# Kernel optimization log

Measured on AMD Instinct MI355X. Metric: run time of the kernel, lower is better.

Reference implementation:

```python
import jax, jax.numpy as jnp
import numpy as np

AMP = 2                      # matches init kwarg `amp`
K = 2 * AMP + 1              # kernel_size


def _offsets():
    # torch: arange(-s//2+1, s//2+1) with s=2*amp+1 -> [-amp, ..., amp]
    vec = jnp.arange(-AMP, AMP + 1, dtype=jnp.float32)
    gi, gj, gs = jnp.meshgrid(vec, vec, vec, indexing='ij')
    # reshape order matches the i-major / j / s-minor loop order below
    return jnp.stack([gi, gj, gs], axis=-1).reshape(K ** 3, 3)  # (K^3, 3)


def setup_inputs() -> dict:
    key = jax.random.key(0)
    k1, k2 = jax.random.split(key)
    B, C, H, W, D = 2, 32, 48, 48, 48
    return {
        "x_q": jax.random.normal(k1, (B, C, H, W, D), dtype=jnp.float32),
        "x_k": jax.random.normal(k2, (B, C, H, W, D), dtype=jnp.float32),
        "num_heads": 4,
    }


def reference(x_q, x_k, num_heads):
    B, C, H, W, D = x_q.shape
    hd = C // num_heads
    scale = hd ** (-0.5)
    q = x_q.reshape(B, hd, num_heads, H, W, D) * scale
    k = x_k.reshape(B, hd, num_heads, H, W, D)

    pad = [(0, 0)] * 3 + [(AMP, AMP)] * 3
    kp = jnp.pad(k, pad)  # zero pad spatial dims by amp
    # validity mask: True inside the original volume, False in the padding
    valid = jnp.pad(jnp.ones((H, W, D), dtype=bool), [(AMP, AMP)] * 3)

    attn = []
    for i in range(K):
        for j in range(K):
            for s in range(K):
                ks = kp[:, :, :, i:i + H, j:j + W, s:s + D]
                # dot over head_dim channel c -> (B, nh, H, W, D)
                a = jnp.einsum('bchxyz,bchxyz->bhxyz', q, ks)
                m = valid[i:i + H, j:j + W, s:s + D]
                attn.append(jnp.where(m, a, jnp.float32(-1000.0)))
    attn = jnp.stack(attn, axis=1)          # (B, K^3, nh, H, W, D)
    attn = jax.nn.softmax(attn, axis=1)     # softmax over the K^3 shifts

    v = _offsets()                          # (K^3, 3)
    v_ = jnp.einsum('bnhxyz,nd->bdhxyz', attn, v)  # (B, 3, nh, H, W, D)
    return jnp.mean(v_, axis=2)             # (B, 3, H, W, D)
```

## Files before the change

### kernel.cpp

```cpp
#include <hip/hip_runtime.h>


#define S_PLANE 2304
#define S_CHAN 110592
#define TOTAL  7077888

typedef _Float16 h2 __attribute__((ext_vector_type(2)));

__device__ __forceinline__ float dot2(h2 a, h2 b, float c) {
#if __has_builtin(__builtin_amdgcn_fdot2)
    return __builtin_amdgcn_fdot2(a, b, c, false);
#else
    return fmaf((float)a[0], (float)b[0], fmaf((float)a[1], (float)b[1], c));
#endif
}

__device__ __forceinline__ float fexp2(float x) {
#if __has_builtin(__builtin_amdgcn_exp2f)
    return __builtin_amdgcn_exp2f(x);
#else
    return __exp2f(x);
#endif
}

__device__ __forceinline__ h2 bc(unsigned w) { return __builtin_bit_cast(h2, w); }

__device__ __forceinline__ unsigned pkz(float a, float b) {
#if __has_builtin(__builtin_amdgcn_cvt_pkrtz)
    return __builtin_bit_cast(unsigned, __builtin_amdgcn_cvt_pkrtz(a, b));
#else
    return __builtin_bit_cast(unsigned, h2{(_Float16)a, (_Float16)b});
#endif
}

__global__ __launch_bounds__(256, 8) void mov3d_kernel(
    const float* __restrict__ xq, const float* __restrict__ xk,
    float* __restrict__ out)
{
    __shared__ __align__(16) unsigned kw[4608];

    const int tid = threadIdx.x;
    const int tz8 = tid & 7;
    const int ty = (tid >> 3) & 7;
    const int tx = tid >> 6;

    const int bid = blockIdx.x;
    int blk = (bid & 7) * 432 + (bid >> 3);

    const int h = blk / 864;
    int rem = blk - h * 864;
    const int zt = rem % 6;  rem /= 6;
    const int yt = rem % 6;  rem /= 6;
    const int xt = rem % 12;
    const int b  = rem / 12;

    const int x0 = xt * 4, y0 = yt * 8, z0 = zt * 8;
    const int x = x0 + tx, y = y0 + ty, z = z0 + tz8;
    const unsigned sp = (unsigned)(x * S_PLANE + y * 48 + z);
    const int bbase = b * (32 * S_CHAN);

    const float QSCALE = 0.35355339059327373f * 1.4426950408889634f;

    const float qf0 = xq[(unsigned)(bbase + (h     ) * S_CHAN) + sp];
    const float qf1 = xq[(unsigned)(bbase + (h +  4) * S_CHAN) + sp];
    const float qf2 = xq[(unsigned)(bbase + (h +  8) * S_CHAN) + sp];
    const float qf3 = xq[(unsigned)(bbase + (h + 12) * S_CHAN) + sp];
    const float qf4 = xq[(unsigned)(bbase + (h + 16) * S_CHAN) + sp];
    const float qf5 = xq[(unsigned)(bbase + (h + 20) * S_CHAN) + sp];
    const float qf6 = xq[(unsigned)(bbase + (h + 24) * S_CHAN) + sp];
    const float qf7 = xq[(unsigned)(bbase + (h + 28) * S_CHAN) + sp];
    const h2 qA0 = h2{(_Float16)(qf0 * QSCALE), (_Float16)(qf1 * QSCALE)};
    const h2 qA1 = h2{(_Float16)(qf2 * QSCALE), (_Float16)(qf3 * QSCALE)};
    const h2 qA2 = h2{(_Float16)(qf4 * QSCALE), (_Float16)(qf5 * QSCALE)};
    const h2 qA3 = h2{(_Float16)(qf6 * QSCALE), (_Float16)(qf7 * QSCALE)};

    const int sBase = bbase + h * S_CHAN;
#define STAGE_GROUP(G) do {                                                   \
        const int u = (G) * 256 + tid;                                        \
        if ((G) < 2 || tid < 64) {                                            \
            const int lx  = u / 72;                                           \
            const int r   = u - lx * 72;                                      \
            const int lz2 = r / 12;                                           \
            const int ly  = r - lz2 * 12;                                     \
            const int srel0 = (x0 - 2 + lx) * S_PLANE                         \
                            + (y0 - 2 + ly) * 48 + (z0 - 2 + 2 * lz2);        \
            const int srel = min(max(srel0, 0), S_CHAN - 2);                  \
            const int f = sBase + srel;     \
            const float2 vA0 = *(const float2*)&xk[f];                        \
            const float2 vA1 = *(const float2*)&xk[f +  8 * S_CHAN];          \
            const float2 vA2 = *(const float2*)&xk[f + 16 * S_CHAN];          \
            const float2 vA3 = *(const float2*)&xk[f + 24 * S_CHAN];          \
            const float2 vB0 = *(const float2*)&xk[f +  4 * S_CHAN];          \
            const float2 vB1 = *(const float2*)&xk[f + 12 * S_CHAN];          \
            const float2 vB2 = *(const float2*)&xk[f + 20 * S_CHAN];          \
            const float2 vB3 = *(const float2*)&xk[f + 28 * S_CHAN];          \
            const uint4 W0 = {pkz(vA0.x, vB0.x), pkz(vA1.x, vB1.x),           \
                              pkz(vA2.x, vB2.x), pkz(vA3.x, vB3.x)};          \
            const uint4 W1 = {pkz(vA0.y, vB0.y), pkz(vA1.y, vB1.y),           \
                              pkz(vA2.y, vB2.y), pkz(vA3.y, vB3.y)};          \
            const int L0 = lx * 144 + lz2 * 24 + ly;                          \
            *(uint4*)&kw[L0 * 4] = W0;                                        \
            *(uint4*)&kw[(L0 + 12) * 4] = W1;                                 \
        }                                                                     \
    } while (0)
    STAGE_GROUP(0);
    STAGE_GROUP(1);
    STAGE_GROUP(2);
#undef STAGE_GROUP
    __syncthreads();

    const float NEG = -16384.f;
    const float zs0 = ((unsigned)(z - 2) < 48u) ? 0.f : NEG;
    const float zs1 = ((unsigned)(z - 1) < 48u) ? 0.f : NEG;
    const float zs2 = 0.f;
    const float zs3 = ((unsigned)(z + 1) < 48u) ? 0.f : NEG;
    const float zs4 = ((unsigned)(z + 2) < 48u) ? 0.f : NEG;

    float l = 0.f, ax = 0.f, ay = 0.f, az = 0.f;

#define SCORE(T, SEED) \
    dot2(qA0, bc((T).x), dot2(qA1, bc((T).y), dot2(qA2, bc((T).z), dot2(qA3, bc((T).w), (SEED)))))

    __builtin_amdgcn_s_setprio(1);
#pragma unroll
    for (int dx = -2; dx <= 2; ++dx) {
        const bool vx = (unsigned)(x + dx) < 48u;
        const float fdx = (float)dx;
        float wsdx = 0.f;
#pragma unroll
        for (int dy = -2; dy <= 2; ++dy) {
            const bool vxy = vx && ((unsigned)(y + dy) < 48u);
            const float fdy = (float)dy;
            const unsigned* pb = kw
                + ((tx + 2 + dx) * 144 + tz8 * 12 + (ty + 2 + dy)) * 4;

            const uint4 T0 = *(const uint4*)(pb);
            const uint4 T1 = *(const uint4*)(pb + 48);
            const uint4 T2 = *(const uint4*)(pb + 96);
            const uint4 T3 = *(const uint4*)(pb + 144);
            const uint4 T4 = *(const uint4*)(pb + 192);

            const float e0 = fexp2(SCORE(T0, zs0));
            const float e1 = fexp2(SCORE(T1, zs1));
            const float e2 = fexp2(SCORE(T2, zs2));
            const float e3 = fexp2(SCORE(T3, zs3));
            const float e4 = fexp2(SCORE(T4, zs4));

            float ws  = ((e0 + e1) + (e2 + e3)) + e4;
            float azP = fmaf(2.f, e4 - e0, e3 - e1);

            ws  = vxy ? ws  : 0.f;
            azP = vxy ? azP : 0.f;

            wsdx += ws;
            ay = fmaf(fdy, ws, ay);
            az += azP;
        }
        ax = fmaf(fdx, wsdx, ax);
        l += wsdx;
    }
    __builtin_amdgcn_s_setprio(0);
#undef SCORE

    const float r = 0.25f / l;
    const unsigned ob = (unsigned)b * (3 * S_CHAN);
    atomicAdd(&out[ob + 0u * S_CHAN + sp], ax * r);
    atomicAdd(&out[ob + 1u * S_CHAN + sp], ay * r);
    atomicAdd(&out[ob + 2u * S_CHAN + sp], az * r);
}

extern "C" void kernel_launch(void* const* d_in, const int* in_sizes, int n_in,
                              void* d_out, int out_size, void* d_ws, size_t ws_size,
                              hipStream_t stream) {
    const float* xq = (const float*)d_in[0];
    const float* xk = (const float*)d_in[1];
    float* out = (float*)d_out;
    hipMemsetAsync(out, 0, (size_t)out_size * sizeof(float), stream);
    mov3d_kernel<<<3456, 256, 0, stream>>>(xq, xk, out);
}
```

Baseline: 50.43 us.

## Compute two z-outputs per thread and enlarge tile to 8x8x8 with padded LDS

Each thread now computes two adjacent z voxels, so the six staged key rows serve both outputs and LDS reads per output drop. The block tile grows from 4x8x8 to 8x8x8, which lowers the share of staged halo per output and halves the grid. The LDS row stride is padded from 144 to 145 to reduce bank conflicts. In exchange it uses more LDS and registers per block (launch bounds lowered to 5 blocks), so occupancy falls and fewer blocks cover the GPU.

Measured after the change: 65.45 us. 29.8% more time.

```diff
diff --git a/kernel.cpp b/kernel.cpp
--- a/kernel.cpp
+++ b/kernel.cpp
@@ -33,51 +33,55 @@
 #endif
 }
 
-__global__ __launch_bounds__(256, 8) void mov3d_kernel(
+__global__ __launch_bounds__(256, 5) void mov3d_kernel(
     const float* __restrict__ xq, const float* __restrict__ xk,
     float* __restrict__ out)
 {
-    __shared__ __align__(16) unsigned kw[4608];
+    __shared__ __align__(16) unsigned kw[6960];
 
     const int tid = threadIdx.x;
-    const int tz8 = tid & 7;
-    const int ty = (tid >> 3) & 7;
-    const int tx = tid >> 6;
+    const int tzi = tid & 3;
+    const int ty = (tid >> 2) & 7;
+    const int tx = tid >> 5;
 
     const int bid = blockIdx.x;
-    int blk = (bid & 7) * 432 + (bid >> 3);
-
-    const int h = blk / 864;
-    int rem = blk - h * 864;
-    const int zt = rem % 6;  rem /= 6;
-    const int yt = rem % 6;  rem /= 6;
-    const int xt = rem % 12;
-    const int b  = rem / 12;
-
-    const int x0 = xt * 4, y0 = yt * 8, z0 = zt * 8;
-    const int x = x0 + tx, y = y0 + ty, z = z0 + tz8;
-    const unsigned sp = (unsigned)(x * S_PLANE + y * 48 + z);
+    int blk = (bid & 7) * 216 + (bid >> 3);
+
+    const int h = blk / 432;
+    int rem = blk - h * 432;
+    const int b = rem / 216;  rem -= b * 216;
+    const int xt = rem / 36;  rem -= xt * 36;
+    const int yt = rem / 6;
+    const int zt = rem - yt * 6;
+
+    const int x0 = xt * 8, y0 = yt * 8, z0 = zt * 8;
+    const int x = x0 + tx, y = y0 + ty, zA = z0 + 2 * tzi;
+    const unsigned sp = (unsigned)(x * S_PLANE + y * 48 + zA);
     const int bbase = b * (32 * S_CHAN);
 
     const float QSCALE = 0.35355339059327373f * 1.4426950408889634f;
 
-    const float qf0 = xq[(unsigned)(bbase + (h     ) * S_CHAN) + sp];
-    const float qf1 = xq[(unsigned)(bbase + (h +  4) * S_CHAN) + sp];
-    const float qf2 = xq[(unsigned)(bbase + (h +  8) * S_CHAN) + sp];
-    const float qf3 = xq[(unsigned)(bbase + (h + 12) * S_CHAN) + sp];
-    const float qf4 = xq[(unsigned)(bbase + (h + 16) * S_CHAN) + sp];
-    const float qf5 = xq[(unsigned)(bbase + (h + 20) * S_CHAN) + sp];
-    const float qf6 = xq[(unsigned)(bbase + (h + 24) * S_CHAN) + sp];
-    const float qf7 = xq[(unsigned)(bbase + (h + 28) * S_CHAN) + sp];
-    const h2 qA0 = h2{(_Float16)(qf0 * QSCALE), (_Float16)(qf1 * QSCALE)};
-    const h2 qA1 = h2{(_Float16)(qf2 * QSCALE), (_Float16)(qf3 * QSCALE)};
-    const h2 qA2 = h2{(_Float16)(qf4 * QSCALE), (_Float16)(qf5 * QSCALE)};
-    const h2 qA3 = h2{(_Float16)(qf6 * QSCALE), (_Float16)(qf7 * QSCALE)};
+    const float2 qf0 = *(const float2*)&xq[(unsigned)(bbase + (h     ) * S_CHAN) + sp];
+    const float2 qf1 = *(const float2*)&xq[(unsigned)(bbase + (h +  4) * S_CHAN) + sp];
+    const float2 qf2 = *(const float2*)&xq[(unsigned)(bbase + (h +  8) * S_CHAN) + sp];
+    const float2 qf3 = *(const float2*)&xq[(unsigned)(bbase + (h + 12) * S_CHAN) + sp];
+    const float2 qf4 = *(const float2*)&xq[(unsigned)(bbase + (h + 16) * S_CHAN) + sp];
+    const float2 qf5 = *(const float2*)&xq[(unsigned)(bbase + (h + 20) * S_CHAN) + sp];
+    const float2 qf6 = *(const float2*)&xq[(unsigned)(bbase + (h + 24) * S_CHAN) + sp];
+    const float2 qf7 = *(const float2*)&xq[(unsigned)(bbase + (h + 28) * S_CHAN) + sp];
+    const h2 qA0 = h2{(_Float16)(qf0.x * QSCALE), (_Float16)(qf1.x * QSCALE)};
+    const h2 qA1 = h2{(_Float16)(qf2.x * QSCALE), (_Float16)(qf3.x * QSCALE)};
+    const h2 qA2 = h2{(_Float16)(qf4.x * QSCALE), (_Float16)(qf5.x * QSCALE)};
+    const h2 qA3 = h2{(_Float16)(qf6.x * QSCALE), (_Float16)(qf7.x * QSCALE)};
+    const h2 qB0 = h2{(_Float16)(qf0.y * QSCALE), (_Float16)(qf1.y * QSCALE)};
+    const h2 qB1 = h2{(_Float16)(qf2.y * QSCALE), (_Float16)(qf3.y * QSCALE)};
+    const h2 qB2 = h2{(_Float16)(qf4.y * QSCALE), (_Float16)(qf5.y * QSCALE)};
+    const h2 qB3 = h2{(_Float16)(qf6.y * QSCALE), (_Float16)(qf7.y * QSCALE)};
 
     const int sBase = bbase + h * S_CHAN;
 #define STAGE_GROUP(G) do {                                                   \
         const int u = (G) * 256 + tid;                                        \
-        if ((G) < 2 || tid < 64) {                                            \
+        if ((G) < 3 || tid < 96) {                                            \
             const int lx  = u / 72;                                           \
             const int r   = u - lx * 72;                                      \
             const int lz2 = r / 12;                                           \
@@ -98,75 +102,95 @@
                               pkz(vA2.x, vB2.x), pkz(vA3.x, vB3.x)};          \
             const uint4 W1 = {pkz(vA0.y, vB0.y), pkz(vA1.y, vB1.y),           \
                               pkz(vA2.y, vB2.y), pkz(vA3.y, vB3.y)};          \
-            const int L0 = lx * 144 + lz2 * 24 + ly;                          \
-            *(uint4*)&kw[L0 * 4] = W0;                                        \
-            *(uint4*)&kw[(L0 + 12) * 4] = W1;                                 \
+            const int L0 = lx * 145 + lz2 * 24 + ly;                          \
+            *(uint4*)&kw[L0 * 4] = W0;                           \
+            *(uint4*)&kw[(L0 + 12) * 4] = W1;                    \
         }                                                                     \
     } while (0)
     STAGE_GROUP(0);
     STAGE_GROUP(1);
     STAGE_GROUP(2);
+    STAGE_GROUP(3);
 #undef STAGE_GROUP
     __syncthreads();
 
     const float NEG = -16384.f;
-    const float zs0 = ((unsigned)(z - 2) < 48u) ? 0.f : NEG;
-    const float zs1 = ((unsigned)(z - 1) < 48u) ? 0.f : NEG;
+    const float zs0 = ((unsigned)(zA - 2) < 48u) ? 0.f : NEG;
+    const float zs1 = ((unsigned)(zA - 1) < 48u) ? 0.f : NEG;
     const float zs2 = 0.f;
-    const float zs3 = ((unsigned)(z + 1) < 48u) ? 0.f : NEG;
-    const float zs4 = ((unsigned)(z + 2) < 48u) ? 0.f : NEG;
-
-    float l = 0.f, ax = 0.f, ay = 0.f, az = 0.f;
-
-#define SCORE(T, SEED) \
+    const float zs3 = ((unsigned)(zA + 1) < 48u) ? 0.f : NEG;
+    const float zs4 = ((unsigned)(zA + 2) < 48u) ? 0.f : NEG;
+    const float zs5 = ((unsigned)(zA + 3) < 48u) ? 0.f : NEG;
+
+    float lA = 0.f, axA = 0.f, ayA = 0.f, azA = 0.f;
+    float lB = 0.f, axB = 0.f, ayB = 0.f, azB = 0.f;
+
+#define SCOREA(T, SEED) \
     dot2(qA0, bc((T).x), dot2(qA1, bc((T).y), dot2(qA2, bc((T).z), dot2(qA3, bc((T).w), (SEED)))))
+#define SCOREB(T, SEED) \
+    dot2(qB0, bc((T).x), dot2(qB1, bc((T).y), dot2(qB2, bc((T).z), dot2(qB3, bc((T).w), (SEED)))))
 
     __builtin_amdgcn_s_setprio(1);
 #pragma unroll
     for (int dx = -2; dx <= 2; ++dx) {
         const bool vx = (unsigned)(x + dx) < 48u;
         const float fdx = (float)dx;
-        float wsdx = 0.f;
+        float wsdxA = 0.f, wsdxB = 0.f;
 #pragma unroll
         for (int dy = -2; dy <= 2; ++dy) {
             const bool vxy = vx && ((unsigned)(y + dy) < 48u);
             const float fdy = (float)dy;
             const unsigned* pb = kw
-                + ((tx + 2 + dx) * 144 + tz8 * 12 + (ty + 2 + dy)) * 4;
+                + ((tx + 2 + dx) * 145 + 2 * tzi * 12 + (ty + 2 + dy)) * 4;
 
             const uint4 T0 = *(const uint4*)(pb);
             const uint4 T1 = *(const uint4*)(pb + 48);
             const uint4 T2 = *(const uint4*)(pb + 96);
             const uint4 T3 = *(const uint4*)(pb + 144);
             const uint4 T4 = *(const uint4*)(pb + 192);
-
-            const float e0 = fexp2(SCORE(T0, zs0));
-            const float e1 = fexp2(SCORE(T1, zs1));
-            const float e2 = fexp2(SCORE(T2, zs2));
-            const float e3 = fexp2(SCORE(T3, zs3));
-            const float e4 = fexp2(SCORE(T4, zs4));
-
-            float ws  = ((e0 + e1) + (e2 + e3)) + e4;
-            float azP = fmaf(2.f, e4 - e0, e3 - e1);
-
-            ws  = vxy ? ws  : 0.f;
-            azP = vxy ? azP : 0.f;
-
-            wsdx += ws;
-            ay = fmaf(fdy, ws, ay);
-            az += azP;
+            const uint4 T5 = *(const uint4*)(pb + 240);
+
+            const float eA0 = fexp2(SCOREA(T0, zs0));
+            const float eA1 = fexp2(SCOREA(T1, zs1));
+            const float eA2 = fexp2(SCOREA(T2, zs2));
+            const float eA3 = fexp2(SCOREA(T3, zs3));
+            const float eA4 = fexp2(SCOREA(T4, zs4));
+            const float eB0 = fexp2(SCOREB(T1, zs1));
+            const float eB1 = fexp2(SCOREB(T2, zs2));
+            const float eB2 = fexp2(SCOREB(T3, zs3));
+            const float eB3 = fexp2(SCOREB(T4, zs4));
+            const float eB4 = fexp2(SCOREB(T5, zs5));
+
+            float wsA  = ((eA0 + eA1) + (eA2 + eA3)) + eA4;
+            float wsB  = ((eB0 + eB1) + (eB2 + eB3)) + eB4;
+            float azPA = fmaf(2.f, eA4 - eA0, eA3 - eA1);
+            float azPB = fmaf(2.f, eB4 - eB0, eB3 - eB1);
+
+            wsA  = vxy ? wsA  : 0.f;
+            wsB  = vxy ? wsB  : 0.f;
+            azPA = vxy ? azPA : 0.f;
+            azPB = vxy ? azPB : 0.f;
+
+            wsdxA += wsA;  wsdxB += wsB;
+            ayA = fmaf(fdy, wsA, ayA);  ayB = fmaf(fdy, wsB, ayB);
+            azA += azPA;  azB += azPB;
         }
-        ax = fmaf(fdx, wsdx, ax);
-        l += wsdx;
+        axA = fmaf(fdx, wsdxA, axA);  axB = fmaf(fdx, wsdxB, axB);
+        lA += wsdxA;  lB += wsdxB;
     }
     __builtin_amdgcn_s_setprio(0);
-#undef SCORE
-
-    const float r = 0.25f / l;
+#undef SCOREA
+#undef SCOREB
+
+    const float rA = 0.25f / lA;
+    const float rB = 0.25f / lB;
     const unsigned ob = (unsigned)b * (3 * S_CHAN);
-    atomicAdd(&out[ob + 0u * S_CHAN + sp], ax * r);
-    atomicAdd(&out[ob + 1u * S_CHAN + sp], ay * r);
-    atomicAdd(&out[ob + 2u * S_CHAN + sp], az * r);
+    atomicAdd(&out[ob + 0u * S_CHAN + sp],     axA * rA);
+    atomicAdd(&out[ob + 0u * S_CHAN + sp + 1], axB * rB);
+    atomicAdd(&out[ob + 1u * S_CHAN + sp],     ayA * rA);
+    atomicAdd(&out[ob + 1u * S_CHAN + sp + 1], ayB * rB);
+    atomicAdd(&out[ob + 2u * S_CHAN + sp],     azA * rA);
+    atomicAdd(&out[ob + 2u * S_CHAN + sp + 1], azB * rB);
 }
 
 extern "C" void kernel_launch(void* const* d_in, const int* in_sizes, int n_in,
@@ -176,5 +200,5 @@
     const float* xk = (const float*)d_in[1];
     float* out = (float*)d_out;
     hipMemsetAsync(out, 0, (size_t)out_size * sizeof(float), stream);
-    mov3d_kernel<<<3456, 256, 0, stream>>>(xq, xk, out);
-}
+    mov3d_kernel<<<1728, 256, 0, stream>>>(xq, xk, out);
+}
```
